# Kernel optimization log

Measured on AMD Instinct MI355X. Metric: run time of the kernel, lower is better.

## Reference

```python
import math
import jax, jax.numpy as jnp
import numpy as np

NUM_ANGLE = 8
NUM_RADIAL = 3
RADIAL_MIN = 0.08
RADIAL_MAX = 0.9
EPS = 1e-6


def _hann(n):
    # torch.hann_window(n, periodic=False)
    return 0.5 * (1.0 - jnp.cos(2.0 * jnp.pi * jnp.arange(n, dtype=jnp.float32) / (n - 1)))


def _to_luma(img):
    # img: [B, 3, H, W] -> [B, H, W]
    return 0.2989 * img[:, 0] + 0.587 * img[:, 1] + 0.114 * img[:, 2]


def _log_magnitude(img):
    x = _to_luma(img).astype(jnp.float32)  # [B, H, W]
    H, W = x.shape[-2], x.shape[-1]
    win = _hann(H)[:, None] * _hann(W)[None, :]  # [H, W]
    x = x * win
    spec = jnp.fft.fftshift(jnp.fft.fft2(x, axes=(-2, -1)), axes=(-2, -1))
    return jnp.log1p(jnp.abs(spec))  # [B, H, W]


def _polar_masks(H, W):
    y = jnp.linspace(-1.0, 1.0, H, dtype=jnp.float32)
    x = jnp.linspace(-1.0, 1.0, W, dtype=jnp.float32)
    yy, xx = jnp.meshgrid(y, x, indexing='ij')
    radius = jnp.sqrt(xx * xx + yy * yy)
    radius = radius / jnp.maximum(radius.max(), EPS)
    angle = jnp.remainder(jnp.arctan2(yy, xx), math.pi)

    r_edges = jnp.linspace(RADIAL_MIN, RADIAL_MAX, NUM_RADIAL + 1, dtype=jnp.float32)
    a_edges = jnp.linspace(0.0, math.pi, NUM_ANGLE + 1, dtype=jnp.float32)

    r0 = r_edges[:-1][:, None, None]
    r1 = r_edges[1:][:, None, None]
    rmask = (radius[None] >= r0) & (radius[None] < r1)           # [R, H, W]
    rmask = rmask.at[-1].set((radius >= r_edges[-2]) & (radius <= r_edges[-1]))

    t0 = a_edges[:-1][:, None, None]
    t1 = a_edges[1:][:, None, None]
    amask = (angle[None] >= t0) & (angle[None] < t1)             # [A, H, W]
    amask = amask.at[-1].set((angle >= a_edges[-2]) & (angle <= a_edges[-1]))

    return (rmask[:, None] & amask[None, :]).astype(jnp.float32)  # [R, A, H, W]


def _sector_energies(img):
    mag = _log_magnitude(img)                          # [B, H, W]
    masks = _polar_masks(mag.shape[-2], mag.shape[-1])  # [R, A, H, W]
    mask_sum = jnp.maximum(masks.sum(axis=(-2, -1)), EPS)        # [R, A]
    masked_sum = jnp.einsum('bhw,rahw->bra', mag, masks)         # [B, R, A]
    energies = masked_sum / mask_sum[None]
    energies = energies / jnp.maximum(energies.sum(axis=-1, keepdims=True), EPS)
    return energies


def setup_inputs() -> dict:
    key = jax.random.key(0)
    k1, k2 = jax.random.split(key)
    B, C, H, W = 16, 3, 512, 512
    prediction = jax.random.uniform(k1, (B, C, H, W), dtype=jnp.float32)
    target = jax.random.uniform(k2, (B, C, H, W), dtype=jnp.float32)
    radial_weights = jnp.array([0.5, 1.0, 1.2], dtype=jnp.float32).reshape(1, NUM_RADIAL, 1)
    return {"prediction": prediction, "target": target, "radial_weights": radial_weights}


def reference(prediction, target, radial_weights):
    pred_e = _sector_energies(prediction)   # [B, R, A]
    tgt_e = _sector_energies(target)
    diff = pred_e - tgt_e
    dist = jnp.sqrt(diff * diff + EPS)      # charbonnier
    return (dist * radial_weights).mean()
```

## Files before the change

### kernel.cpp

```cpp
#include <hip/hip_runtime.h>
#include <math.h>

#define PI_F 3.14159265358979323846f
#define TWO_PI_F 6.28318530717958647692f
#define RSQ2 0.70710678118654752440f

#define WAVE_SYNC() __asm__ volatile("s_waitcnt lgkmcnt(0)" ::: "memory")
#define LADDR(a) ((a) + ((a) >> 3))

__device__ __forceinline__ float2 cadd(float2 a, float2 b){ return make_float2(a.x+b.x, a.y+b.y); }
__device__ __forceinline__ float2 csub(float2 a, float2 b){ return make_float2(a.x-b.x, a.y-b.y); }
__device__ __forceinline__ float2 cmul(float2 a, float2 b){ return make_float2(a.x*b.x - a.y*b.y, a.x*b.y + a.y*b.x); }
__device__ __forceinline__ float2 cw1(float2 a){ return make_float2(RSQ2*(a.x+a.y), RSQ2*(a.y-a.x)); }
__device__ __forceinline__ float2 cw2(float2 a){ return make_float2(a.y, -a.x); }
__device__ __forceinline__ float2 cw3(float2 a){ return make_float2(RSQ2*(a.y-a.x), -RSQ2*(a.x+a.y)); }

__device__ __forceinline__ void dft8(float2* v){
    float2 a0=cadd(v[0],v[4]), a1=cadd(v[1],v[5]), a2=cadd(v[2],v[6]), a3=cadd(v[3],v[7]);
    float2 b0=csub(v[0],v[4]);
    float2 b1=cw1(csub(v[1],v[5]));
    float2 b2=cw2(csub(v[2],v[6]));
    float2 b3=cw3(csub(v[3],v[7]));
    float2 c0=cadd(a0,a2), c2=csub(a0,a2), c1=cadd(a1,a3), c3=cw2(csub(a1,a3));
    float2 d0=cadd(b0,b2), d2=csub(b0,b2), d1=cadd(b1,b3), d3=cw2(csub(b1,b3));
    v[0]=cadd(c0,c1); v[1]=csub(c0,c1);
    v[2]=cadd(c2,c3); v[3]=csub(c2,c3);
    v[4]=cadd(d0,d1); v[5]=csub(d0,d1);
    v[6]=cadd(d2,d3); v[7]=csub(d2,d3);
}

__device__ __forceinline__ void stage_store(float2* wl, const float2* v, float2 w1,
                                            int base, int step){
    constexpr int br[8] = {0,4,2,6,1,5,3,7};
    wl[LADDR(base)] = v[0];
    float2 p = w1;
    #pragma unroll
    for (int c = 1; c < 8; ++c) {
        wl[LADDR(base + step*c)] = cmul(v[br[c]], p);
        p = cmul(p, w1);
    }
}

__device__ __forceinline__ void stage_load(const float2* wl, float2* v, int j){
    #pragma unroll
    for (int i = 0; i < 8; ++i) v[i] = wl[LADDR(j + 64*i)];
}

__device__ __forceinline__ int sector_id(int hm, int wm) {
    const float step = 2.0f / 511.0f;
    float y = -1.0f + step * (float)hm;
    float x = -1.0f + step * (float)wm;
    float radius = sqrtf(x * x + y * y);
    float r = radius / sqrtf(2.0f);
    float a = atan2f(y, x);
    a = fmodf(a, PI_F);
    if (a < 0.0f) a += PI_F;

    const float rstep = (0.9f - 0.08f) / 3.0f;
    const float re0 = 0.08f;
    const float re1 = 0.08f + rstep;
    const float re2 = 0.08f + 2.0f * rstep;
    const float re3 = 0.9f;
    int rb;
    if      (r >= re0 && r < re1)  rb = 0;
    else if (r >= re1 && r < re2)  rb = 1;
    else if (r >= re2 && r <= re3) rb = 2;
    else return -1;

    const float astep = PI_F / 8.0f;
    int ab = 7;
    #pragma unroll
    for (int i = 0; i < 7; ++i) {
        float t0 = astep * (float)i;
        float t1 = astep * (float)(i + 1);
        if (a >= t0 && a < t1) { ab = i; break; }
    }
    return rb * 8 + ab;
}

__device__ __forceinline__ float hannf(int i) {
    return 0.5f * (1.0f - __cosf(TWO_PI_F * (float)i / 511.0f));
}

__global__ __launch_bounds__(256) void rowfft_kernel(const float* __restrict__ pred,
                                                     const float* __restrict__ tgt,
                                                     float4* __restrict__ out4,
                                                     unsigned char* __restrict__ mapT,
                                                     unsigned char* __restrict__ cnt_u8,
                                                     float* __restrict__ acc_rep) {
    __shared__ float2 lds[4 * 576];
    __shared__ float cbins[24];
    int blk = blockIdx.x;
    int img = blk >> 6;
    int pb  = blk & 63;
    int t = threadIdx.x;
    int wv = t >> 6, j = t & 63;
    int hp = pb * 4 + wv;
    int h0 = 2 * hp;
    float2* wl = lds + wv * 576;

    if (blk < 48) acc_rep[blk * 256 + t] = 0.0f;
    if (t < 24) cbins[t] = 0.0f;
    __syncthreads();
    if (t < 128) {
        int idx = blk * 128 + t;
        int wm = idx >> 9, hm = idx & 511;
        int s = sector_id(hm, wm);
        mapT[idx] = (unsigned char)(s < 0 ? 255 : s);
        if (s >= 0) atomicAdd(&cbins[s], 1.0f);
    }

    const float* base = (img < 16) ? (pred + (size_t)img * 786432)
                                   : (tgt  + (size_t)(img - 16) * 786432);
    float wh0 = hannf(h0), wh1 = hannf(h0 + 1);
    float2 v[8];
    #pragma unroll
    for (int i = 0; i < 8; ++i) {
        int w = j + 64 * i;
        float ww = hannf(w);
        size_t off0 = (size_t)h0 * 512 + w;
        size_t off1 = off0 + 512;
        float l0 = 0.2989f*base[off0] + 0.587f*base[off0+262144] + 0.114f*base[off0+524288];
        float l1 = 0.2989f*base[off1] + 0.587f*base[off1+262144] + 0.114f*base[off1+524288];
        v[i] = make_float2(l0 * (wh0 * ww), l1 * (wh1 * ww));
    }
    float sn, cs;
    dft8(v);
    __sincosf(-TWO_PI_F * (float)j / 512.0f, &sn, &cs);
    stage_store(wl, v, make_float2(cs, sn), 8 * j, 1);
    WAVE_SYNC();
    stage_load(wl, v, j);
    WAVE_SYNC();
    dft8(v);
    __sincosf(-TWO_PI_F * (float)((j >> 3) << 3) / 512.0f, &sn, &cs);
    stage_store(wl, v, make_float2(cs, sn), (j & 7) + 64 * (j >> 3), 8);
    WAVE_SYNC();
    stage_load(wl, v, j);
    dft8(v);
    constexpr int br[8] = {0,4,2,6,1,5,3,7};
    size_t kbase = (size_t)img * 256;
    int partner = (64 - j) & 63;
    #pragma unroll
    for (int c = 0; c < 4; ++c) {
        float2 zk = v[br[c]];
        float mx = __shfl(v[br[7 - c]].x, partner, 64);
        float my = __shfl(v[br[7 - c]].y, partner, 64);
        float2 zs = v[br[(8 - c) & 7]];
        float2 zm = make_float2(j == 0 ? zs.x : mx, j == 0 ? zs.y : my);
        int k = j + 64 * c;
        float4 o = make_float4(0.5f*(zk.x+zm.x), 0.5f*(zk.y-zm.y),
                               0.5f*(zk.y+zm.y), 0.5f*(zm.x-zk.x));
        if (k != 0) out4[(kbase + (size_t)k) * 256 + hp] = o;
    }
    if (j == 0) {
        float2 z0 = v[br[0]], z4 = v[br[4]];
        out4[kbase * 256 + hp] = make_float4(z0.x, z4.x, z0.y, z4.y);
    }
    __syncthreads();
    if (t < 24) cnt_u8[t * 2048 + blk] = (unsigned char)(int)cbins[t];
}

__global__ __launch_bounds__(256, 8) void colfft_kernel(const float2* __restrict__ buf,
                                                        const unsigned char* __restrict__ mapT,
                                                        float* __restrict__ acc_rep) {
    __shared__ float2 lds[4 * 576];
    int t = threadIdx.x;
    int wv = t >> 6, j = t & 63;
    int gid = blockIdx.x * 4 + wv;
    int img = gid >> 8;
    int widx = gid & 255;
    float2* wl = lds + wv * 576;

    const float2* col = buf + (size_t)gid * 512;
    float2 v[8];
    #pragma unroll
    for (int i = 0; i < 8; ++i) v[i] = col[j + 64 * i];

    bool pairw = (widx == 0);
    const unsigned char* mwA = mapT + (size_t)(pairw ? 256 : ((widx + 256) & 511)) * 512;
    const unsigned char* mwB = mapT + (size_t)(pairw ? 0   : ((256 - widx) & 511)) * 512;
    unsigned char sA[8], sB[8];
    #pragma unroll
    for (int c = 0; c < 8; ++c) {
        int hm = j + 64 * ((c + 4) & 7);
        sA[c] = mwA[hm];
        int hm2 = pairw ? hm : ((256 - (j + 64 * c)) & 511);
        sB[c] = mwB[hm2];
    }

    float sn, cs;
    dft8(v);
    __sincosf(-TWO_PI_F * (float)j / 512.0f, &sn, &cs);
    stage_store(wl, v, make_float2(cs, sn), 8 * j, 1);
    WAVE_SYNC();
    stage_load(wl, v, j);
    WAVE_SYNC();
    dft8(v);
    __sincosf(-TWO_PI_F * (float)((j >> 3) << 3) / 512.0f, &sn, &cs);
    stage_store(wl, v, make_float2(cs, sn), (j & 7) + 64 * (j >> 3), 8);
    WAVE_SYNC();
    stage_load(wl, v, j);
    dft8(v);
    WAVE_SYNC();
    float* wb = (float*)wl;
    #pragma unroll
    for (int i = 0; i < 4; ++i) { int ii = j + 64 * i; if (ii < 200) wb[ii] = 0.0f; }
    WAVE_SYNC();

    constexpr int br[8] = {0,4,2,6,1,5,3,7};
    int rep = (j & 7) * 25;
    if (pairw) {
        int partner = (64 - j) & 63;
        #pragma unroll
        for (int c = 0; c < 8; ++c) {
            float2 zk = v[br[c]];
            float mx = __shfl(v[br[7 - c]].x, partner, 64);
            float my = __shfl(v[br[7 - c]].y, partner, 64);
            float2 zs = v[br[(8 - c) & 7]];
            float2 zm = make_float2(j == 0 ? zs.x : mx, j == 0 ? zs.y : my);
            float f0x = 0.5f*(zk.x+zm.x), f0y = 0.5f*(zk.y-zm.y);
            float f1x = 0.5f*(zk.y+zm.y), f1y = 0.5f*(zm.x-zk.x);
            float mag0 = log1pf(sqrtf(f0x*f0x + f0y*f0y));
            float mag1 = log1pf(sqrtf(f1x*f1x + f1y*f1y));
            int s1 = sA[c]; if (s1 < 24) atomicAdd(&wb[rep + s1], mag0);
            int s2 = sB[c]; if (s2 < 24) atomicAdd(&wb[rep + s2], mag1);
        }
    } else {
        #pragma unroll
        for (int c = 0; c < 8; ++c) {
            float2 z = v[br[c]];
            float mag = log1pf(sqrtf(z.x * z.x + z.y * z.y));
            int s1 = sA[c]; if (s1 < 24) atomicAdd(&wb[rep + s1], mag);
            int s2 = sB[c]; if (s2 < 24) atomicAdd(&wb[rep + s2], mag);
        }
    }
    WAVE_SYNC();
    if (j < 24) {
        float sum = 0.0f;
        #pragma unroll
        for (int r = 0; r < 8; ++r) sum += wb[r * 25 + j];
        atomicAdd(&acc_rep[(gid & 15) * 768 + img * 24 + j], sum);
    }
}

__global__ __launch_bounds__(256) void final_kernel(const float* __restrict__ acc_rep,
                                                    const unsigned char* __restrict__ cnt_u8,
                                                    const float* __restrict__ rw,
                                                    float* __restrict__ out) {
    __shared__ float accs[768];
    __shared__ float cnts[24];
    __shared__ float ep[384], et[384], red[384];
    int t = threadIdx.x;
    for (int o = t; o < 768; o += 256) {
        float s = 0.0f;
        #pragma unroll
        for (int r = 0; r < 16; ++r) s += acc_rep[r * 768 + o];
        accs[o] = s;
    }
    if (t < 192) {
        int s = t >> 3, g = t & 7;
        const uchar4* p = (const uchar4*)(cnt_u8 + s * 2048 + g * 256);
        float sum = 0.0f;
        #pragma unroll
        for (int i = 0; i < 64; ++i) { uchar4 u = p[i]; sum += (float)(u.x + u.y + u.z + u.w); }
        sum += __shfl_down(sum, 4, 8);
        sum += __shfl_down(sum, 2, 8);
        sum += __shfl_down(sum, 1, 8);
        if (g == 0) cnts[s] = sum;
    }
    __syncthreads();
    for (int idx = t; idx < 384; idx += 256) {
        int b = idx / 24, s = idx - b * 24;
        float cnt = fmaxf(cnts[s], 1e-6f);
        ep[idx] = accs[b * 24 + s] / cnt;
        et[idx] = accs[(16 + b) * 24 + s] / cnt;
    }
    __syncthreads();
    for (int idx = t; idx < 384; idx += 256) {
        int b = idx / 24, s = idx - b * 24, r = s >> 3;
        int gbase = b * 24 + r * 8;
        float sp = 0.0f, st = 0.0f;
        #pragma unroll
        for (int a = 0; a < 8; ++a) { sp += ep[gbase + a]; st += et[gbase + a]; }
        float pe = ep[idx] / fmaxf(sp, 1e-6f);
        float te = et[idx] / fmaxf(st, 1e-6f);
        float d = pe - te;
        red[idx] = sqrtf(d * d + 1e-6f) * rw[r];
    }
    __syncthreads();
    if (t < 128) red[t] += red[t + 128] + red[t + 256];
    __syncthreads();
    if (t < 64) {
        float vv = red[t] + red[t + 64];
        #pragma unroll
        for (int o = 32; o > 0; o >>= 1) vv += __shfl_down(vv, o, 64);
        if (t == 0) out[0] = vv / 384.0f;
    }
}

extern "C" void kernel_launch(void* const* d_in, const int* in_sizes, int n_in,
                              void* d_out, int out_size, void* d_ws, size_t ws_size,
                              hipStream_t stream) {
    const float* pred = (const float*)d_in[0];
    const float* tgt  = (const float*)d_in[1];
    const float* rw   = (const float*)d_in[2];

    char* ws = (char*)d_ws;
    float* acc_rep      = (float*)ws;
    unsigned char* cnt  = (unsigned char*)(ws + 49152);
    unsigned char* mapT = (unsigned char*)(ws + 98304);
    float2* buf         = (float2*)(ws + 360448);

    rowfft_kernel<<<2048, 256, 0, stream>>>(pred, tgt, (float4*)buf, mapT, cnt, acc_rep);
    colfft_kernel<<<2048, 256, 0, stream>>>(buf, mapT, acc_rep);
    final_kernel<<<1, 256, 0, stream>>>(acc_rep, cnt, rw, (float*)d_out);
}
```

Before: 203.3 us.

## Process two FFT row/column pairs per wavefront with interleaved LDS stages

Each wavefront in the row and column FFT kernels now handles two independent 512-point transforms instead of one. Their LDS stores, loads and butterflies are interleaved under partial lgkmcnt waits, so LDS latency is hidden behind the other transform's math. Twiddle powers are precomputed once per stage rather than chained per element. Grid sizes are halved, launch bounds drop to 4 blocks/CU, and LDS and register use per block double. Also swaps log1pf for __logf(1+x) and widens the per-block count buffer to 16 bits.

```diff
diff --git a/kernel.cpp b/kernel.cpp
--- a/kernel.cpp
+++ b/kernel.cpp
@@ -5,7 +5,7 @@
 #define TWO_PI_F 6.28318530717958647692f
 #define RSQ2 0.70710678118654752440f
 
-#define WAVE_SYNC() __asm__ volatile("s_waitcnt lgkmcnt(0)" ::: "memory")
+#define LGKM(n) __asm__ volatile("s_waitcnt lgkmcnt(" #n ")" ::: "memory")
 #define LADDR(a) ((a) + ((a) >> 3))
 
 __device__ __forceinline__ float2 cadd(float2 a, float2 b){ return make_float2(a.x+b.x, a.y+b.y); }
@@ -29,16 +29,22 @@
     v[6]=cadd(d2,d3); v[7]=csub(d2,d3);
 }
 
-__device__ __forceinline__ void stage_store(float2* wl, const float2* v, float2 w1,
+__device__ __forceinline__ void calc_pows(float2 w, float2* p){
+    p[0] = w;
+    p[1] = cmul(w, w);
+    p[2] = cmul(p[1], w);
+    p[3] = cmul(p[1], p[1]);
+    p[4] = cmul(p[2], p[1]);
+    p[5] = cmul(p[2], p[2]);
+    p[6] = cmul(p[3], p[2]);
+}
+
+__device__ __forceinline__ void stage_store(float2* wl, const float2* v, const float2* p,
                                             int base, int step){
     constexpr int br[8] = {0,4,2,6,1,5,3,7};
     wl[LADDR(base)] = v[0];
-    float2 p = w1;
-    #pragma unroll
-    for (int c = 1; c < 8; ++c) {
-        wl[LADDR(base + step*c)] = cmul(v[br[c]], p);
-        p = cmul(p, w1);
-    }
+    #pragma unroll
+    for (int c = 1; c < 8; ++c) wl[LADDR(base + step*c)] = cmul(v[br[c]], p[c-1]);
 }
 
 __device__ __forceinline__ void stage_load(const float2* wl, float2* v, int j){
@@ -82,28 +88,34 @@
     return 0.5f * (1.0f - __cosf(TWO_PI_F * (float)i / 511.0f));
 }
 
-__global__ __launch_bounds__(256) void rowfft_kernel(const float* __restrict__ pred,
-                                                     const float* __restrict__ tgt,
-                                                     float4* __restrict__ out4,
-                                                     unsigned char* __restrict__ mapT,
-                                                     unsigned char* __restrict__ cnt_u8,
-                                                     float* __restrict__ acc_rep) {
-    __shared__ float2 lds[4 * 576];
+__device__ __forceinline__ float lumaf(const float* b, size_t off){
+    return 0.2989f*b[off] + 0.587f*b[off+262144] + 0.114f*b[off+524288];
+}
+
+__global__ __launch_bounds__(256, 4) void rowfft_kernel(const float* __restrict__ pred,
+                                                        const float* __restrict__ tgt,
+                                                        float4* __restrict__ out4,
+                                                        unsigned char* __restrict__ mapT,
+                                                        unsigned short* __restrict__ cnt_u16,
+                                                        float* __restrict__ acc_rep) {
+    __shared__ float2 lds[4 * 1152];
     __shared__ float cbins[24];
     int blk = blockIdx.x;
-    int img = blk >> 6;
-    int pb  = blk & 63;
+    int img = blk >> 5;
+    int pb  = blk & 31;
     int t = threadIdx.x;
     int wv = t >> 6, j = t & 63;
-    int hp = pb * 4 + wv;
-    int h0 = 2 * hp;
-    float2* wl = lds + wv * 576;
+    int hpA = pb * 8 + wv * 2;
+    int hpB = hpA + 1;
+    int h0 = 2 * hpA;
+    float2* wlA = lds + wv * 1152;
+    float2* wlB = wlA + 576;
 
     if (blk < 48) acc_rep[blk * 256 + t] = 0.0f;
     if (t < 24) cbins[t] = 0.0f;
     __syncthreads();
-    if (t < 128) {
-        int idx = blk * 128 + t;
+    {
+        int idx = blk * 256 + t;
         int wm = idx >> 9, hm = idx & 511;
         int s = sector_id(hm, wm);
         mapT[idx] = (unsigned char)(s < 0 ? 255 : s);
@@ -112,100 +124,159 @@
 
     const float* base = (img < 16) ? (pred + (size_t)img * 786432)
                                    : (tgt  + (size_t)(img - 16) * 786432);
-    float wh0 = hannf(h0), wh1 = hannf(h0 + 1);
-    float2 v[8];
+    float whA0 = hannf(h0), whA1 = hannf(h0 + 1);
+    float whB0 = hannf(h0 + 2), whB1 = hannf(h0 + 3);
+    float2 va[8], vb[8];
     #pragma unroll
     for (int i = 0; i < 8; ++i) {
         int w = j + 64 * i;
         float ww = hannf(w);
         size_t off0 = (size_t)h0 * 512 + w;
-        size_t off1 = off0 + 512;
-        float l0 = 0.2989f*base[off0] + 0.587f*base[off0+262144] + 0.114f*base[off0+524288];
-        float l1 = 0.2989f*base[off1] + 0.587f*base[off1+262144] + 0.114f*base[off1+524288];
-        v[i] = make_float2(l0 * (wh0 * ww), l1 * (wh1 * ww));
-    }
+        float l0 = lumaf(base, off0);
+        float l1 = lumaf(base, off0 + 512);
+        float l2 = lumaf(base, off0 + 1024);
+        float l3 = lumaf(base, off0 + 1536);
+        va[i] = make_float2(l0 * (whA0 * ww), l1 * (whA1 * ww));
+        vb[i] = make_float2(l2 * (whB0 * ww), l3 * (whB1 * ww));
+    }
+
     float sn, cs;
-    dft8(v);
     __sincosf(-TWO_PI_F * (float)j / 512.0f, &sn, &cs);
-    stage_store(wl, v, make_float2(cs, sn), 8 * j, 1);
-    WAVE_SYNC();
-    stage_load(wl, v, j);
-    WAVE_SYNC();
-    dft8(v);
+    float2 tw0 = make_float2(cs, sn);
     __sincosf(-TWO_PI_F * (float)((j >> 3) << 3) / 512.0f, &sn, &cs);
-    stage_store(wl, v, make_float2(cs, sn), (j & 7) + 64 * (j >> 3), 8);
-    WAVE_SYNC();
-    stage_load(wl, v, j);
-    dft8(v);
+    float2 tw1 = make_float2(cs, sn);
+    float2 pw[7];
+
+    calc_pows(tw0, pw);
+    dft8(va);
+    dft8(vb);
+    stage_store(wlA, va, pw, 8 * j, 1);
+    stage_store(wlB, vb, pw, 8 * j, 1);
+    LGKM(8);
+    stage_load(wlA, va, j);
+    LGKM(8);
+    stage_load(wlB, vb, j);
+    LGKM(8);
+    calc_pows(tw1, pw);
+    dft8(va);
+    stage_store(wlA, va, pw, (j & 7) + 64 * (j >> 3), 8);
+    LGKM(8);
+    dft8(vb);
+    stage_store(wlB, vb, pw, (j & 7) + 64 * (j >> 3), 8);
+    LGKM(8);
+    stage_load(wlA, va, j);
+    LGKM(8);
+    stage_load(wlB, vb, j);
+    LGKM(8);
+    dft8(va);
+    LGKM(0);
+    dft8(vb);
+
     constexpr int br[8] = {0,4,2,6,1,5,3,7};
     size_t kbase = (size_t)img * 256;
     int partner = (64 - j) & 63;
     #pragma unroll
     for (int c = 0; c < 4; ++c) {
-        float2 zk = v[br[c]];
-        float mx = __shfl(v[br[7 - c]].x, partner, 64);
-        float my = __shfl(v[br[7 - c]].y, partner, 64);
-        float2 zs = v[br[(8 - c) & 7]];
+        int k = j + 64 * c;
+        float2 zk = va[br[c]];
+        float mx = __shfl(va[br[7 - c]].x, partner, 64);
+        float my = __shfl(va[br[7 - c]].y, partner, 64);
+        float2 zs = va[br[(8 - c) & 7]];
         float2 zm = make_float2(j == 0 ? zs.x : mx, j == 0 ? zs.y : my);
-        int k = j + 64 * c;
         float4 o = make_float4(0.5f*(zk.x+zm.x), 0.5f*(zk.y-zm.y),
                                0.5f*(zk.y+zm.y), 0.5f*(zm.x-zk.x));
-        if (k != 0) out4[(kbase + (size_t)k) * 256 + hp] = o;
+        if (k != 0) out4[(kbase + (size_t)k) * 256 + hpA] = o;
+        zk = vb[br[c]];
+        mx = __shfl(vb[br[7 - c]].x, partner, 64);
+        my = __shfl(vb[br[7 - c]].y, partner, 64);
+        zs = vb[br[(8 - c) & 7]];
+        zm = make_float2(j == 0 ? zs.x : mx, j == 0 ? zs.y : my);
+        o = make_float4(0.5f*(zk.x+zm.x), 0.5f*(zk.y-zm.y),
+                        0.5f*(zk.y+zm.y), 0.5f*(zm.x-zk.x));
+        if (k != 0) out4[(kbase + (size_t)k) * 256 + hpB] = o;
     }
     if (j == 0) {
-        float2 z0 = v[br[0]], z4 = v[br[4]];
-        out4[kbase * 256 + hp] = make_float4(z0.x, z4.x, z0.y, z4.y);
-    }
-    __syncthreads();
-    if (t < 24) cnt_u8[t * 2048 + blk] = (unsigned char)(int)cbins[t];
-}
-
-__global__ __launch_bounds__(256, 8) void colfft_kernel(const float2* __restrict__ buf,
+        float2 z0 = va[br[0]], z4 = va[br[4]];
+        out4[kbase * 256 + hpA] = make_float4(z0.x, z4.x, z0.y, z4.y);
+        z0 = vb[br[0]]; z4 = vb[br[4]];
+        out4[kbase * 256 + hpB] = make_float4(z0.x, z4.x, z0.y, z4.y);
+    }
+    __syncthreads();
+    if (t < 24) cnt_u16[t * 1024 + blk] = (unsigned short)(int)cbins[t];
+}
+
+__global__ __launch_bounds__(256, 4) void colfft_kernel(const float2* __restrict__ buf,
                                                         const unsigned char* __restrict__ mapT,
                                                         float* __restrict__ acc_rep) {
-    __shared__ float2 lds[4 * 576];
+    __shared__ float2 lds[4 * 1152];
     int t = threadIdx.x;
     int wv = t >> 6, j = t & 63;
-    int gid = blockIdx.x * 4 + wv;
-    int img = gid >> 8;
-    int widx = gid & 255;
-    float2* wl = lds + wv * 576;
-
-    const float2* col = buf + (size_t)gid * 512;
-    float2 v[8];
-    #pragma unroll
-    for (int i = 0; i < 8; ++i) v[i] = col[j + 64 * i];
-
-    bool pairw = (widx == 0);
-    const unsigned char* mwA = mapT + (size_t)(pairw ? 256 : ((widx + 256) & 511)) * 512;
-    const unsigned char* mwB = mapT + (size_t)(pairw ? 0   : ((256 - widx) & 511)) * 512;
-    unsigned char sA[8], sB[8];
+    int pg = blockIdx.x * 4 + wv;
+    int gidA = pg * 2;
+    int img = pg >> 7;
+    int wA = gidA & 255, wB = wA + 1;
+    float2* wlA = lds + wv * 1152;
+    float2* wlB = wlA + 576;
+
+    const float2* colA = buf + (size_t)gidA * 512;
+    float2 va[8], vb[8];
+    #pragma unroll
+    for (int i = 0; i < 8; ++i) va[i] = colA[j + 64 * i];
+    #pragma unroll
+    for (int i = 0; i < 8; ++i) vb[i] = colA[512 + j + 64 * i];
+
+    bool pairw = (wA == 0);
+    const unsigned char* mwA1 = mapT + (size_t)(pairw ? 256 : ((wA + 256) & 511)) * 512;
+    const unsigned char* mwA2 = mapT + (size_t)(pairw ? 0   : ((256 - wA) & 511)) * 512;
+    const unsigned char* mwB1 = mapT + (size_t)((wB + 256) & 511) * 512;
+    const unsigned char* mwB2 = mapT + (size_t)((256 - wB) & 511) * 512;
+    unsigned char sA1[8], sA2[8], sB1[8], sB2[8];
     #pragma unroll
     for (int c = 0; c < 8; ++c) {
         int hm = j + 64 * ((c + 4) & 7);
-        sA[c] = mwA[hm];
-        int hm2 = pairw ? hm : ((256 - (j + 64 * c)) & 511);
-        sB[c] = mwB[hm2];
+        int hm2 = (256 - (j + 64 * c)) & 511;
+        sA1[c] = mwA1[hm];
+        sA2[c] = pairw ? mwA2[hm] : mwA2[hm2];
+        sB1[c] = mwB1[hm];
+        sB2[c] = mwB2[hm2];
     }
 
     float sn, cs;
-    dft8(v);
     __sincosf(-TWO_PI_F * (float)j / 512.0f, &sn, &cs);
-    stage_store(wl, v, make_float2(cs, sn), 8 * j, 1);
-    WAVE_SYNC();
-    stage_load(wl, v, j);
-    WAVE_SYNC();
-    dft8(v);
+    float2 tw0 = make_float2(cs, sn);
     __sincosf(-TWO_PI_F * (float)((j >> 3) << 3) / 512.0f, &sn, &cs);
-    stage_store(wl, v, make_float2(cs, sn), (j & 7) + 64 * (j >> 3), 8);
-    WAVE_SYNC();
-    stage_load(wl, v, j);
-    dft8(v);
-    WAVE_SYNC();
-    float* wb = (float*)wl;
+    float2 tw1 = make_float2(cs, sn);
+    float2 pw[7];
+
+    calc_pows(tw0, pw);
+    dft8(va);
+    dft8(vb);
+    stage_store(wlA, va, pw, 8 * j, 1);
+    stage_store(wlB, vb, pw, 8 * j, 1);
+    LGKM(8);
+    stage_load(wlA, va, j);
+    LGKM(8);
+    stage_load(wlB, vb, j);
+    LGKM(8);
+    calc_pows(tw1, pw);
+    dft8(va);
+    stage_store(wlA, va, pw, (j & 7) + 64 * (j >> 3), 8);
+    LGKM(8);
+    dft8(vb);
+    stage_store(wlB, vb, pw, (j & 7) + 64 * (j >> 3), 8);
+    LGKM(8);
+    stage_load(wlA, va, j);
+    LGKM(8);
+    stage_load(wlB, vb, j);
+    LGKM(8);
+    dft8(va);
+    LGKM(0);
+    dft8(vb);
+
+    float* wb = (float*)wlA;
     #pragma unroll
     for (int i = 0; i < 4; ++i) { int ii = j + 64 * i; if (ii < 200) wb[ii] = 0.0f; }
-    WAVE_SYNC();
+    LGKM(0);
 
     constexpr int br[8] = {0,4,2,6,1,5,3,7};
     int rep = (j & 7) * 25;
@@ -213,38 +284,45 @@
         int partner = (64 - j) & 63;
         #pragma unroll
         for (int c = 0; c < 8; ++c) {
-            float2 zk = v[br[c]];
-            float mx = __shfl(v[br[7 - c]].x, partner, 64);
-            float my = __shfl(v[br[7 - c]].y, partner, 64);
-            float2 zs = v[br[(8 - c) & 7]];
+            float2 zk = va[br[c]];
+            float mx = __shfl(va[br[7 - c]].x, partner, 64);
+            float my = __shfl(va[br[7 - c]].y, partner, 64);
+            float2 zs = va[br[(8 - c) & 7]];
             float2 zm = make_float2(j == 0 ? zs.x : mx, j == 0 ? zs.y : my);
             float f0x = 0.5f*(zk.x+zm.x), f0y = 0.5f*(zk.y-zm.y);
             float f1x = 0.5f*(zk.y+zm.y), f1y = 0.5f*(zm.x-zk.x);
-            float mag0 = log1pf(sqrtf(f0x*f0x + f0y*f0y));
-            float mag1 = log1pf(sqrtf(f1x*f1x + f1y*f1y));
-            int s1 = sA[c]; if (s1 < 24) atomicAdd(&wb[rep + s1], mag0);
-            int s2 = sB[c]; if (s2 < 24) atomicAdd(&wb[rep + s2], mag1);
+            float mag0 = __logf(1.0f + sqrtf(f0x*f0x + f0y*f0y));
+            float mag1 = __logf(1.0f + sqrtf(f1x*f1x + f1y*f1y));
+            int s1 = sA1[c]; if (s1 < 24) atomicAdd(&wb[rep + s1], mag0);
+            int s2 = sA2[c]; if (s2 < 24) atomicAdd(&wb[rep + s2], mag1);
         }
     } else {
         #pragma unroll
         for (int c = 0; c < 8; ++c) {
-            float2 z = v[br[c]];
-            float mag = log1pf(sqrtf(z.x * z.x + z.y * z.y));
-            int s1 = sA[c]; if (s1 < 24) atomicAdd(&wb[rep + s1], mag);
-            int s2 = sB[c]; if (s2 < 24) atomicAdd(&wb[rep + s2], mag);
+            float2 z = va[br[c]];
+            float mag = __logf(1.0f + sqrtf(z.x * z.x + z.y * z.y));
+            int s1 = sA1[c]; if (s1 < 24) atomicAdd(&wb[rep + s1], mag);
+            int s2 = sA2[c]; if (s2 < 24) atomicAdd(&wb[rep + s2], mag);
         }
     }
-    WAVE_SYNC();
+    #pragma unroll
+    for (int c = 0; c < 8; ++c) {
+        float2 z = vb[br[c]];
+        float mag = __logf(1.0f + sqrtf(z.x * z.x + z.y * z.y));
+        int s1 = sB1[c]; if (s1 < 24) atomicAdd(&wb[rep + s1], mag);
+        int s2 = sB2[c]; if (s2 < 24) atomicAdd(&wb[rep + s2], mag);
+    }
+    LGKM(0);
     if (j < 24) {
         float sum = 0.0f;
         #pragma unroll
         for (int r = 0; r < 8; ++r) sum += wb[r * 25 + j];
-        atomicAdd(&acc_rep[(gid & 15) * 768 + img * 24 + j], sum);
+        atomicAdd(&acc_rep[(pg & 15) * 768 + img * 24 + j], sum);
     }
 }
 
 __global__ __launch_bounds__(256) void final_kernel(const float* __restrict__ acc_rep,
-                                                    const unsigned char* __restrict__ cnt_u8,
+                                                    const unsigned short* __restrict__ cnt_u16,
                                                     const float* __restrict__ rw,
                                                     float* __restrict__ out) {
     __shared__ float accs[768];
@@ -259,10 +337,10 @@
     }
     if (t < 192) {
         int s = t >> 3, g = t & 7;
-        const uchar4* p = (const uchar4*)(cnt_u8 + s * 2048 + g * 256);
+        const ushort4* p = (const ushort4*)(cnt_u16 + s * 1024 + g * 128);
         float sum = 0.0f;
         #pragma unroll
-        for (int i = 0; i < 64; ++i) { uchar4 u = p[i]; sum += (float)(u.x + u.y + u.z + u.w); }
+        for (int i = 0; i < 32; ++i) { ushort4 u = p[i]; sum += (float)(u.x + u.y + u.z + u.w); }
         sum += __shfl_down(sum, 4, 8);
         sum += __shfl_down(sum, 2, 8);
         sum += __shfl_down(sum, 1, 8);
@@ -306,12 +384,12 @@
     const float* rw   = (const float*)d_in[2];
 
     char* ws = (char*)d_ws;
-    float* acc_rep      = (float*)ws;
-    unsigned char* cnt  = (unsigned char*)(ws + 49152);
-    unsigned char* mapT = (unsigned char*)(ws + 98304);
-    float2* buf         = (float2*)(ws + 360448);
-
-    rowfft_kernel<<<2048, 256, 0, stream>>>(pred, tgt, (float4*)buf, mapT, cnt, acc_rep);
-    colfft_kernel<<<2048, 256, 0, stream>>>(buf, mapT, acc_rep);
+    float* acc_rep       = (float*)ws;
+    unsigned short* cnt  = (unsigned short*)(ws + 49152);
+    unsigned char* mapT  = (unsigned char*)(ws + 98304);
+    float2* buf          = (float2*)(ws + 360448);
+
+    rowfft_kernel<<<1024, 256, 0, stream>>>(pred, tgt, (float4*)buf, mapT, cnt, acc_rep);
+    colfft_kernel<<<1024, 256, 0, stream>>>(buf, mapT, acc_rep);
     final_kernel<<<1, 256, 0, stream>>>(acc_rep, cnt, rw, (float*)d_out);
 }
```

Result: faster. 194.3 us (-4.5%).
